# Performance work log

Measured on AMD Instinct MI355X. Metric: run time of the kernel, lower is better.

Reference implementation:

```python
import jax, jax.numpy as jnp
import numpy as np

B, L, D, H = 2, 2048, 1024, 16
DH = D // H  # 64

def setup_inputs() -> dict:
    key = jax.random.key(0)
    ks = jax.random.split(key, 5)
    s = 1.0 / np.sqrt(D)
    return {
        "x": jax.random.normal(ks[0], (B, L, D), jnp.float32),
        "Wk": jax.random.normal(ks[1], (D, D), jnp.float32) * s,
        "Wq": jax.random.normal(ks[2], (D, D), jnp.float32) * s,
        "Wv": jax.random.normal(ks[3], (D, D), jnp.float32) * s,
        "Wo": jax.random.normal(ks[4], (D, D), jnp.float32) * s,
    }

def reference(x, Wk, Wq, Wv, Wo):
    # Linear(D,D,bias=False): y = x @ W.T ; W stored [out,in] as in torch
    k = (x @ Wk.T).reshape(B, L, H, DH).transpose(0, 2, 1, 3)  # [B,H,L,dh]
    q = (x @ Wq.T).reshape(B, L, H, DH).transpose(0, 2, 1, 3)
    v = (x @ Wv.T).reshape(B, L, H, DH).transpose(0, 2, 1, 3)
    att = jnp.einsum("bhqd,bhkd->bhqk", q, k) / jnp.sqrt(jnp.float32(DH))
    causal = jnp.tril(jnp.ones((L, L), dtype=bool))
    att = jnp.where(causal, att, -jnp.inf)
    p = jax.nn.softmax(att, axis=-1)  # dropout omitted (eval mode)
    out = jnp.einsum("bhqk,bhkd->bhqd", p, v)  # [B,H,L,dh]
    out = out.transpose(0, 2, 1, 3).reshape(B, L, D)
    return out @ Wo.T
```

## Files before the change

### kernel.cpp

```cpp
#include <hip/hip_runtime.h>

typedef __bf16 bf16_t;
typedef __bf16 bf16x8 __attribute__((ext_vector_type(8)));
typedef __bf16 bf16x4 __attribute__((ext_vector_type(4)));
typedef float f32x4 __attribute__((ext_vector_type(4)));

#define MFMA_BF16(a, b, c) __builtin_amdgcn_mfma_f32_16x16x32_bf16((a), (b), (c), 0, 0, 0)
#define LOG2E 1.44269504088896f

__device__ __forceinline__ void gload16(const bf16_t* g, bf16_t* l) {
  __builtin_amdgcn_global_load_lds(
      (__attribute__((address_space(1))) void*)(g),
      (__attribute__((address_space(3))) void*)(l), 16, 0, 0);
}

__global__ void cast_all(const float* __restrict__ x, const float* __restrict__ wk,
                         const float* __restrict__ wq, const float* __restrict__ wv,
                         const float* __restrict__ wo, bf16_t* __restrict__ xbf,
                         bf16_t* __restrict__ wbf) {
  const size_t NX = 4194304, NW = 1048576;
  size_t i = (size_t)blockIdx.x * blockDim.x + threadIdx.x;
  const size_t total4 = (NX + 4 * NW) / 4;
  const size_t stride = (size_t)gridDim.x * blockDim.x;
  for (; i < total4; i += stride) {
    size_t f = i * 4;
    const float* src;
    bf16_t* dst;
    if (f < NX) {
      src = x + f;
      dst = xbf + f;
    } else {
      size_t g = f - NX;
      size_t wsel = g >> 20;
      size_t off = g & (NW - 1);
      dst = wbf + g;
      src = (wsel == 0) ? wq + off : (wsel == 1) ? wk + off : (wsel == 2) ? wv + off : wo + off;
    }
    float4 v = *(const float4*)src;
    bf16x4 o;
    o[0] = (bf16_t)v.x; o[1] = (bf16_t)v.y; o[2] = (bf16_t)v.z; o[3] = (bf16_t)v.w;
    *(bf16x4*)dst = o;
  }
}

template <int BM, int BN, typename TOUT>
__global__ __launch_bounds__(256) void gemm_nt(const bf16_t* __restrict__ A,
                                               const bf16_t* __restrict__ W,
                                               TOUT* __restrict__ C, int K, int ldc,
                                               int blocksPerSect, bf16_t* __restrict__ vtb) {
  constexpr int MF = BM / 32;
  constexpr int NF = BN / 32;
  constexpr int ABYTES = BM * 128;
  constexpr int BBYTES = BN * 128;
  __shared__ bf16_t As[2][BM * 64];
  __shared__ bf16_t Bs[2][BN * 64];
  const int t = threadIdx.x;
  const int l = t & 63, w = t >> 6;
  const int wm = w >> 1;
  const int wn = w & 1;
  const int lr = l & 15, lg = l >> 4;
  const int bm = blockIdx.x;
  const int by = blockIdx.y;
  const int sect = by / blocksPerSect;
  const int bn = by - sect * blocksPerSect;
  const bf16_t* Wp = W + ((size_t)sect << 20);
  const int n0 = sect * 1024 + bn * BN;

  const int srow0 = t >> 3;
  const int csw = (t & 7) ^ (srow0 & 7);
  const bf16_t* ag = A + (size_t)(bm * BM + srow0) * K + csw * 8;
  const bf16_t* bg = Wp + (size_t)(bn * BN + srow0) * K + csw * 8;
  char* As0 = (char*)&As[0][0];
  char* Bs0 = (char*)&Bs[0][0];
  const int stg = t * 16;

#define GSTAGE(k0, sb)                                                                             \
  do {                                                                                             \
    _Pragma("unroll") for (int p = 0; p < BM / 32; ++p)                                            \
        gload16(ag + (size_t)(32 * p) * K + (k0), (bf16_t*)(As0 + (sb) * ABYTES + p * 4096 + stg)); \
    _Pragma("unroll") for (int p = 0; p < BN / 32; ++p)                                            \
        gload16(bg + (size_t)(32 * p) * K + (k0), (bf16_t*)(Bs0 + (sb) * BBYTES + p * 4096 + stg)); \
  } while (0)

  const int r7 = lr & 7;
  const int o0 = lr * 128 + ((lg ^ r7) * 16);
  const int abase = wm * (MF * 2048) + o0;
  const int bbase = wn * (NF * 2048) + o0;

  f32x4 acc[MF][NF];
#pragma unroll
  for (int i = 0; i < MF; ++i)
#pragma unroll
    for (int j = 0; j < NF; ++j) acc[i][j] = (f32x4){0.f, 0.f, 0.f, 0.f};

  GSTAGE(0, 0);
  __syncthreads();

  int cb = 0;
  for (int k0 = 0; k0 < K; k0 += 64) {
    if (k0 + 64 < K) GSTAGE(k0 + 64, cb ^ 1);
#pragma unroll
    for (int kk = 0; kk < 2; ++kk) {
      bf16x8 af[MF], bfr[NF];
#pragma unroll
      for (int mf = 0; mf < MF; ++mf)
        af[mf] = *(const bf16x8*)(As0 + cb * ABYTES + ((abase + mf * 2048) ^ (kk * 64)));
#pragma unroll
      for (int nf = 0; nf < NF; ++nf)
        bfr[nf] = *(const bf16x8*)(Bs0 + cb * BBYTES + ((bbase + nf * 2048) ^ (kk * 64)));
#pragma unroll
      for (int mf = 0; mf < MF; ++mf)
#pragma unroll
        for (int nf = 0; nf < NF; ++nf)
          acc[mf][nf] = MFMA_BF16(af[mf], bfr[nf], acc[mf][nf]);
    }
    __syncthreads();
    cb ^= 1;
  }
#undef GSTAGE

  if (vtb != nullptr && sect == 2) {
#pragma unroll
    for (int mf = 0; mf < MF; ++mf)
#pragma unroll
      for (int nf = 0; nf < NF; ++nf) {
        int row0 = bm * BM + wm * (MF * 16) + mf * 16 + lg * 4;
        int colg = bn * BN + wn * (NF * 16) + nf * 16 + lr;
        int bb = row0 >> 11, ll = row0 & 2047;
        size_t vaddr = ((size_t)((bb * 16 + (colg >> 6)) * 64 + (colg & 63))) * 2048 + ll;
        bf16x4 pk;
#pragma unroll
        for (int j = 0; j < 4; ++j) pk[j] = (bf16_t)acc[mf][nf][j];
        *(bf16x4*)(vtb + vaddr) = pk;
      }
    return;
  }
#pragma unroll
  for (int mf = 0; mf < MF; ++mf)
#pragma unroll
    for (int nf = 0; nf < NF; ++nf)
#pragma unroll
      for (int j = 0; j < 4; ++j) {
        int row = bm * BM + wm * (MF * 16) + mf * 16 + lg * 4 + j;
        int col = n0 + wn * (NF * 16) + nf * 16 + lr;
        C[(size_t)row * ldc + col] = (TOUT)acc[mf][nf][j];
      }
}

__global__ __launch_bounds__(512, 4) void attn_fwd(const bf16_t* __restrict__ qk,
                                                   const bf16_t* __restrict__ vt,
                                                   bf16_t* __restrict__ out) {
  __shared__ bf16_t Ks[2][8192];
  __shared__ bf16_t Vts[2][8192];
  __shared__ bf16_t Pt[8][1024];
  const int t = threadIdx.x, l = t & 63, w = t >> 6;
  const int lr = l & 15, lg = l >> 4;
  const int n = blockIdx.x;
  const int bh = n & 31;
  const int b = bh >> 4, h = bh & 15;
  const int pr = n >> 5;
  const int qlo = pr, qhi = 31 - pr;
  const int part = w >> 2;
  const int wq4 = w & 3;
  const int qt = part ? qlo : qhi;
  const int qloc = wq4 * 16 + lr;
  const int qrow = qt * 64 + qloc;

  const float SCINIT = -12.f * LOG2E;

  const int srow = t >> 3, sc8 = t & 7;
  const int cs = sc8 ^ (srow & 7);
  const bf16_t* kbase = qk + ((size_t)(b * 2048 + srow)) * 2048 + 1024 + h * 64 + cs * 8;
  const bf16_t* vbase = vt + ((size_t)(bh * 64 + srow)) * 2048 + cs * 8;
  char* Ks0 = (char*)&Ks[0][0];
  char* Vt0 = (char*)&Vts[0][0];
  const int stg = t * 16;

#define STAGE(pair, sboff)                                             \
  do {                                                                 \
    const bf16_t* ks_ = kbase + (size_t)(pair) * (128 * 2048);         \
    const bf16_t* vs_ = vbase + (size_t)(pair) * 128;                  \
    gload16(ks_, (bf16_t*)(Ks0 + (sboff) + stg));                      \
    gload16(ks_ + (size_t)64 * 2048, (bf16_t*)(Ks0 + (sboff) + 8192 + stg)); \
    gload16(vs_, (bf16_t*)(Vt0 + (sboff) + stg));                      \
    gload16(vs_ + 64, (bf16_t*)(Vt0 + (sboff) + 8192 + stg));          \
  } while (0)

  const float qsc = 0.125f * LOG2E;
  const bf16_t* Qg = qk + (size_t)(b * 2048 + qrow) * 2048 + h * 64 + lg * 8;
  bf16x8 qf0 = *(const bf16x8*)(Qg);
  bf16x8 qf1 = *(const bf16x8*)(Qg + 32);
#pragma unroll
  for (int jj = 0; jj < 8; ++jj) {
    qf0[jj] = (bf16_t)((float)qf0[jj] * qsc);
    qf1[jj] = (bf16_t)((float)qf1[jj] * qsc);
  }

  f32x4 acc[4];
#pragma unroll
  for (int df = 0; df < 4; ++df) acc[df] = (f32x4){0.f, 0.f, 0.f, 0.f};
  float l_r = 0.f;

  const int r7 = lr & 7;
  const int o0 = lr * 128 + ((lg ^ r7) * 16);
  const int o1 = lr * 128 + (((lg ^ 4) ^ r7) * 16);

  char* PwB = (char*)&Pt[w][0];
  const int psw = r7 << 4;
  int pwo[4];
#pragma unroll
  for (int nf = 0; nf < 4; ++nf) pwo[nf] = lr * 128 + ((nf * 32 + lg * 8) ^ psw);
  const int pr0 = lr * 128 + ((lg * 16) ^ psw);
  const int pr1 = lr * 128 + ((64 + lg * 16) ^ psw);

  STAGE(0, 0);
  __syncthreads();

  const int itMax = qhi >> 1;
  int boff = 0;
  for (int it = 0; it <= itMax; ++it) {
    if (it < itMax) STAGE(it + 1, boff ^ 16384);

#pragma unroll
    for (int s = 0; s < 2; ++s) {
      const int kt = 2 * it + s;
      if (kt <= qt) {
        const int sub = boff + s * 8192;
        f32x4 sc[4];
#pragma unroll
        for (int nf = 0; nf < 4; ++nf)
          sc[nf] = (f32x4){SCINIT, SCINIT, SCINIT, SCINIT};
        __builtin_amdgcn_s_setprio(1);
#pragma unroll
        for (int nf = 0; nf < 4; ++nf) {
          bf16x8 kf0 = *(const bf16x8*)(Ks0 + sub + nf * 2048 + o0);
          bf16x8 kf1 = *(const bf16x8*)(Ks0 + sub + nf * 2048 + o1);
          sc[nf] = MFMA_BF16(kf0, qf0, sc[nf]);
          sc[nf] = MFMA_BF16(kf1, qf1, sc[nf]);
        }
        __builtin_amdgcn_s_setprio(0);

        float p[16], ps = 0.f;
        if (kt == qt) {
#pragma unroll
          for (int nf = 0; nf < 4; ++nf)
#pragma unroll
            for (int jj = 0; jj < 4; ++jj) {
              float sv = sc[nf][jj];
              if (nf * 16 + lg * 4 + jj > qloc) sv = -1e30f;
              float pv = __builtin_amdgcn_exp2f(sv);
              p[nf * 4 + jj] = pv;
              ps += pv;
            }
        } else {
#pragma unroll
          for (int nf = 0; nf < 4; ++nf)
#pragma unroll
            for (int jj = 0; jj < 4; ++jj) {
              float pv = __builtin_amdgcn_exp2f(sc[nf][jj]);
              p[nf * 4 + jj] = pv;
              ps += pv;
            }
        }
        l_r += ps;

#pragma unroll
        for (int nf = 0; nf < 4; ++nf) {
          bf16x4 pk;
#pragma unroll
          for (int jj = 0; jj < 4; ++jj) pk[jj] = (bf16_t)p[nf * 4 + jj];
          *(bf16x4*)(PwB + pwo[nf]) = pk;
        }

        bf16x8 pb0 = *(const bf16x8*)(PwB + pr0);
        bf16x8 pb1 = *(const bf16x8*)(PwB + pr1);
        __builtin_amdgcn_s_setprio(1);
#pragma unroll
        for (int df = 0; df < 4; ++df) {
          bf16x8 vf0 = *(const bf16x8*)(Vt0 + sub + df * 2048 + o0);
          bf16x8 vf1 = *(const bf16x8*)(Vt0 + sub + df * 2048 + o1);
          acc[df] = MFMA_BF16(vf0, pb0, acc[df]);
          acc[df] = MFMA_BF16(vf1, pb1, acc[df]);
        }
        __builtin_amdgcn_s_setprio(0);
      }
    }
    __syncthreads();
    boff ^= 16384;
  }
#undef STAGE

  l_r += __shfl_xor(l_r, 16);
  l_r += __shfl_xor(l_r, 32);
  float inv = 1.f / l_r;
#pragma unroll
  for (int df = 0; df < 4; ++df) {
    bf16x4 o;
#pragma unroll
    for (int jj = 0; jj < 4; ++jj) o[jj] = (bf16_t)(acc[df][jj] * inv);
    *(bf16x4*)(out + (size_t)(b * 2048 + qrow) * 1024 + h * 64 + df * 16 + lg * 4) = o;
  }
}

extern "C" void kernel_launch(void* const* d_in, const int* in_sizes, int n_in,
                              void* d_out, int out_size, void* d_ws, size_t ws_size,
                              hipStream_t stream) {
  const float* x = (const float*)d_in[0];
  const float* wk = (const float*)d_in[1];
  const float* wq = (const float*)d_in[2];
  const float* wv = (const float*)d_in[3];
  const float* wo = (const float*)d_in[4];

  bf16_t* xbf = (bf16_t*)d_ws;
  bf16_t* wbf = xbf + 4194304;
  bf16_t* qkbf = wbf + 4194304;
  bf16_t* vtbuf = qkbf + 8388608;
  bf16_t* attnbf = xbf;
  float* out = (float*)d_out;

  cast_all<<<dim3(2048), dim3(256), 0, stream>>>(x, wk, wq, wv, wo, xbf, wbf);
  gemm_nt<128, 64, bf16_t><<<dim3(32, 48), dim3(256), 0, stream>>>(xbf, wbf, qkbf, 1024, 2048, 16,
                                                                   vtbuf);
  attn_fwd<<<dim3(512), dim3(512), 0, stream>>>(qkbf, vtbuf, attnbf);
  gemm_nt<64, 64, float><<<dim3(64, 16), dim3(256), 0, stream>>>(attnbf, wbf + 3 * 1048576, out,
                                                                 1024, 1024, 16, (bf16_t*)nullptr);
}
```

Before: 96.46 us.

## Add dedicated QKV GEMM kernel with triple-buffered 32-wide K pipeline

Replaces the generic gemm_nt used for the QKV projection with a specialized kernel that streams 32-wide K slices through a three-stage LDS ring buffer and uses explicit vmcnt waits with a single barrier per iteration. It also sets launch bounds to allow four blocks per CU, using smaller LDS tiles. The aim is to hide global-to-LDS latency better and raise occupancy, in exchange for more barriers and k-iterations with less MFMA work per sync.

```diff
diff --git a/kernel.cpp b/kernel.cpp
--- a/kernel.cpp
+++ b/kernel.cpp
@@ -43,11 +43,121 @@
   }
 }
 
+__global__ __launch_bounds__(256, 4) void gemm_qkv(const bf16_t* __restrict__ A,
+                                                   const bf16_t* __restrict__ W,
+                                                   bf16_t* __restrict__ C,
+                                                   bf16_t* __restrict__ vtb) {
+  constexpr int K = 1024;
+  __shared__ bf16_t As[3][128 * 32];
+  __shared__ bf16_t Bs[3][64 * 32];
+  const int t = threadIdx.x;
+  const int l = t & 63, w = t >> 6;
+  const int wm = w >> 1, wn = w & 1;
+  const int lr = l & 15, lg = l >> 4;
+  const int bm = blockIdx.x;
+  const int by = blockIdx.y;
+  const int sect = by >> 4;
+  const int bn = by & 15;
+  const bf16_t* Wp = W + ((size_t)sect << 20);
+  const int n0 = sect * 1024 + bn * 64;
+
+  const int srow0 = t >> 2;
+  const int csw = (t & 3) ^ ((t >> 3) & 3);
+  const bf16_t* ag = A + (size_t)(bm * 128 + srow0) * K + csw * 8;
+  const bf16_t* bg = Wp + (size_t)(bn * 64 + srow0) * K + csw * 8;
+  char* As0 = (char*)&As[0][0];
+  char* Bs0 = (char*)&Bs[0][0];
+  const int stg = t * 16;
+
+#define QSTAGE(k0, sb)                                                          \
+  do {                                                                          \
+    gload16(ag + (k0), (bf16_t*)(As0 + (sb) * 8192 + stg));                     \
+    gload16(ag + (size_t)64 * K + (k0), (bf16_t*)(As0 + (sb) * 8192 + 4096 + stg)); \
+    gload16(bg + (k0), (bf16_t*)(Bs0 + (sb) * 4096 + stg));                     \
+  } while (0)
+
+  const int off = lr * 64 + ((lg ^ ((lr >> 1) & 3)) * 16);
+  const int abase = wm * 4096 + off;
+  const int bbase = wn * 2048 + off;
+
+  f32x4 acc[4][2];
+#pragma unroll
+  for (int i = 0; i < 4; ++i)
+#pragma unroll
+    for (int j = 0; j < 2; ++j) acc[i][j] = (f32x4){0.f, 0.f, 0.f, 0.f};
+
+  QSTAGE(0, 0);
+  QSTAGE(32, 1);
+  asm volatile("s_waitcnt vmcnt(3)" ::: "memory");
+  __builtin_amdgcn_s_barrier();
+  __builtin_amdgcn_sched_barrier(0);
+
+  int cb = 0;
+  for (int k0 = 0; k0 < K; k0 += 32) {
+    const bool pf = (k0 + 64 < K);
+    if (pf) {
+      int nb = cb + 2;
+      if (nb >= 3) nb -= 3;
+      QSTAGE(k0 + 64, nb);
+    }
+    bf16x8 af[4], bfr[2];
+#pragma unroll
+    for (int mf = 0; mf < 4; ++mf)
+      af[mf] = *(const bf16x8*)(As0 + cb * 8192 + abase + mf * 1024);
+#pragma unroll
+    for (int nf = 0; nf < 2; ++nf)
+      bfr[nf] = *(const bf16x8*)(Bs0 + cb * 4096 + bbase + nf * 1024);
+#pragma unroll
+    for (int mf = 0; mf < 4; ++mf)
+#pragma unroll
+      for (int nf = 0; nf < 2; ++nf)
+        acc[mf][nf] = MFMA_BF16(af[mf], bfr[nf], acc[mf][nf]);
+    if (k0 + 32 < K) {
+      if (pf)
+        asm volatile("s_waitcnt vmcnt(3)" ::: "memory");
+      else
+        asm volatile("s_waitcnt vmcnt(0)" ::: "memory");
+      __builtin_amdgcn_s_barrier();
+      __builtin_amdgcn_sched_barrier(0);
+    }
+    ++cb;
+    if (cb >= 3) cb = 0;
+  }
+#undef QSTAGE
+
+  if (sect == 2) {
+#pragma unroll
+    for (int mf = 0; mf < 4; ++mf)
+#pragma unroll
+      for (int nf = 0; nf < 2; ++nf) {
+        int row0 = bm * 128 + wm * 64 + mf * 16 + lg * 4;
+        int colg = bn * 64 + wn * 32 + nf * 16 + lr;
+        int bb = row0 >> 11, ll = row0 & 2047;
+        size_t vaddr = ((size_t)((bb * 16 + (colg >> 6)) * 64 + (colg & 63))) * 2048 + ll;
+        bf16x4 pk;
+#pragma unroll
+        for (int j = 0; j < 4; ++j) pk[j] = (bf16_t)acc[mf][nf][j];
+        *(bf16x4*)(vtb + vaddr) = pk;
+      }
+    return;
+  }
+#pragma unroll
+  for (int mf = 0; mf < 4; ++mf)
+#pragma unroll
+    for (int nf = 0; nf < 2; ++nf)
+#pragma unroll
+      for (int j = 0; j < 4; ++j) {
+        int row = bm * 128 + wm * 64 + mf * 16 + lg * 4 + j;
+        int col = n0 + wn * 32 + nf * 16 + lr;
+        C[(size_t)row * 2048 + col] = acc[mf][nf][j];
+      }
+}
+
 template <int BM, int BN, typename TOUT>
 __global__ __launch_bounds__(256) void gemm_nt(const bf16_t* __restrict__ A,
                                                const bf16_t* __restrict__ W,
                                                TOUT* __restrict__ C, int K, int ldc,
-                                               int blocksPerSect, bf16_t* __restrict__ vtb) {
+                                               int blocksPerSect) {
   constexpr int MF = BM / 32;
   constexpr int NF = BN / 32;
   constexpr int ABYTES = BM * 128;
@@ -119,22 +229,6 @@
   }
 #undef GSTAGE
 
-  if (vtb != nullptr && sect == 2) {
-#pragma unroll
-    for (int mf = 0; mf < MF; ++mf)
-#pragma unroll
-      for (int nf = 0; nf < NF; ++nf) {
-        int row0 = bm * BM + wm * (MF * 16) + mf * 16 + lg * 4;
-        int colg = bn * BN + wn * (NF * 16) + nf * 16 + lr;
-        int bb = row0 >> 11, ll = row0 & 2047;
-        size_t vaddr = ((size_t)((bb * 16 + (colg >> 6)) * 64 + (colg & 63))) * 2048 + ll;
-        bf16x4 pk;
-#pragma unroll
-        for (int j = 0; j < 4; ++j) pk[j] = (bf16_t)acc[mf][nf][j];
-        *(bf16x4*)(vtb + vaddr) = pk;
-      }
-    return;
-  }
 #pragma unroll
   for (int mf = 0; mf < MF; ++mf)
 #pragma unroll
@@ -319,9 +413,8 @@
   float* out = (float*)d_out;
 
   cast_all<<<dim3(2048), dim3(256), 0, stream>>>(x, wk, wq, wv, wo, xbf, wbf);
-  gemm_nt<128, 64, bf16_t><<<dim3(32, 48), dim3(256), 0, stream>>>(xbf, wbf, qkbf, 1024, 2048, 16,
-                                                                   vtbuf);
+  gemm_qkv<<<dim3(32, 48), dim3(256), 0, stream>>>(xbf, wbf, qkbf, vtbuf);
   attn_fwd<<<dim3(512), dim3(512), 0, stream>>>(qkbf, vtbuf, attnbf);
   gemm_nt<64, 64, float><<<dim3(64, 16), dim3(256), 0, stream>>>(attnbf, wbf + 3 * 1048576, out,
-                                                                 1024, 1024, 16, (bf16_t*)nullptr);
-}
+                                                                 1024, 1024, 16);
+}
```

Result: slower. 104.4 us (+8.2%).
